# Optimization experiments

Hardware: AMD Instinct MI355X
Metric: run time of the kernel (lower is better)

Reference implementation:

```python
import jax, jax.numpy as jnp
import numpy as np

B, C, S, DC, P, VOCAB = 32, 2048, 512, 128, 768, 32000
CHARS_PER_SUB = C // S  # contiguous non-overlapping spans, no zero-width offsets


def setup_inputs() -> dict:
    key = jax.random.key(0)
    k1, k2, k3 = jax.random.split(key, 3)
    char_sequences = jax.random.randint(k1, (B, C), 0, VOCAB, dtype=jnp.int64 if jax.config.jax_enable_x64 else jnp.int32)
    # offsets[b, p] = (start, end) char span of subword p: contiguous spans of width 4
    starts = jnp.arange(S, dtype=jnp.int32) * CHARS_PER_SUB
    ends = starts + CHARS_PER_SUB
    offsets = jnp.broadcast_to(jnp.stack([starts, ends], axis=-1), (B, S, 2))
    char_table = jax.random.normal(k2, (VOCAB, DC), dtype=jnp.float32)
    pretrained_embeddings = jax.random.normal(k3, (B, S, P), dtype=jnp.float32)
    return {
        "char_sequences": char_sequences,
        "offsets": offsets,
        "char_table": char_table,
        "pretrained_embeddings": pretrained_embeddings,
    }


def _scatter_subword_to_chars(starts, ends, sub):
    # starts, ends: [S]; sub: [S, P]. For char position k, find p with start<=k<end.
    pos = jnp.arange(C)
    idx = jnp.clip(jnp.searchsorted(starts, pos, side="right") - 1, 0, starts.shape[0] - 1)
    valid = (pos >= starts[idx]) & (pos < ends[idx])  # positions not covered get zeros
    return jnp.where(valid[:, None], sub[idx], jnp.zeros((), sub.dtype))  # [C, P]


def reference(char_sequences, offsets, char_table, pretrained_embeddings):
    # character embedding lookup (dropout p=0.0 is identity)
    char_emb = char_table[char_sequences]  # [B, C, DC]
    scattered = jax.vmap(_scatter_subword_to_chars)(
        offsets[..., 0], offsets[..., 1], pretrained_embeddings
    )  # [B, C, P]
    return jnp.concatenate([char_emb, scattered], axis=-1)  # [B, C, DC+P]
```

## Files before the change

kernel.cpp:

```cpp
#include <hip/hip_runtime.h>
#include <stdint.h>

#define SCAT_THREADS (32u * 512u * 192u)
#define CHAR_CHUNKS  (32u * 2048u * 32u)

typedef float f32x4 __attribute__((ext_vector_type(4)));

__global__ __launch_bounds__(256) void EmbeddingLayer_14516989460967_kernel(
    const int*   __restrict__ seq,
    const int*   __restrict__ offsets,
    const float* __restrict__ table,
    const float* __restrict__ pret,
    float*       __restrict__ out)
{
    uint32_t gtid = blockIdx.x * 256u + threadIdx.x;

    if (gtid < SCAT_THREADS) {
        uint32_t sp  = gtid / 192u;
        uint32_t ck  = gtid - sp * 192u;
        int2 se = *(const int2*)(offsets + (sp << 1));
        f32x4 v = *(const f32x4*)(pret + (size_t)sp * 768u + (ck << 2));
        uint32_t b  = sp >> 9;
        uint32_t c0 = (sp & 511u) << 2;
        float* dst = out + ((size_t)((b << 11) + c0)) * 896u + 128u + (ck << 2);
        const f32x4 z = {0.f, 0.f, 0.f, 0.f};
#pragma unroll
        for (int j = 0; j < 4; ++j) {
            int c = (int)c0 + j;
            f32x4 w = (c >= se.x && c < se.y) ? v : z;
            *(f32x4*)(dst + (size_t)j * 896u) = w;
        }
    } else {
        uint32_t cid = gtid - SCAT_THREADS;
        uint32_t row = cid >> 5;
        uint32_t col = (cid & 31u) << 2;
        int tok = seq[row];
        f32x4 v = *(const f32x4*)(table + (size_t)tok * 128u + col);
        *(f32x4*)(out + (size_t)row * 896u + col) = v;
    }
}

extern "C" void kernel_launch(void* const* d_in, const int* in_sizes, int n_in,
                              void* d_out, int out_size, void* d_ws, size_t ws_size,
                              hipStream_t stream) {
    const int*   seq     = (const int*)  d_in[0];
    const int*   offsets = (const int*)  d_in[1];
    const float* table   = (const float*)d_in[2];
    const float* pret    = (const float*)d_in[3];

    uint32_t total_threads = SCAT_THREADS + CHAR_CHUNKS;
    uint32_t blocks = total_threads / 256u;
    EmbeddingLayer_14516989460967_kernel<<<blocks, 256, 0, stream>>>(
        seq, offsets, table, pret, (float*)d_out);
}
```

Before: 54.27 us.

## Assign each block a contiguous 16-row output tile covering both segments

Each block now handles 16 consecutive output rows (4 subwords) and writes both the char-embedding columns and the scattered subword columns for them, instead of two separate thread ranges writing the two segments in distant parts of the grid. The aim is to make each block's writes cover whole contiguous rows so DRAM write locality improves, and to cut the block count. Each thread now does more work (2 gather chunks plus 3 scatter chunks), so there is less parallelism to hide latency, and the block count is hardcoded to these sizes.

```diff
diff --git a/kernel.cpp b/kernel.cpp
--- a/kernel.cpp
+++ b/kernel.cpp
@@ -1,10 +1,10 @@
 #include <hip/hip_runtime.h>
 #include <stdint.h>
 
-#define SCAT_THREADS (32u * 512u * 192u)
-#define CHAR_CHUNKS  (32u * 2048u * 32u)
 
 typedef float f32x4 __attribute__((ext_vector_type(4)));
+
+#define NBLOCKS 4096u
 
 __global__ __launch_bounds__(256) void EmbeddingLayer_14516989460967_kernel(
     const int*   __restrict__ seq,
@@ -13,30 +13,37 @@
     const float* __restrict__ pret,
     float*       __restrict__ out)
 {
-    uint32_t gtid = blockIdx.x * 256u + threadIdx.x;
+    const uint32_t tid = threadIdx.x;
+    const uint32_t r0  = blockIdx.x * 16u;
+    const uint32_t sp0 = blockIdx.x * 4u;
 
-    if (gtid < SCAT_THREADS) {
-        uint32_t sp  = gtid / 192u;
-        uint32_t ck  = gtid - sp * 192u;
+#pragma unroll
+    for (uint32_t k = 0; k < 2u; ++k) {
+        uint32_t ci  = k * 256u + tid;
+        uint32_t row = r0 + (ci >> 5);
+        uint32_t col = (ci & 31u) << 2;
+        int tok = seq[row];
+        f32x4 v = *(const f32x4*)(table + (size_t)tok * 128u + col);
+        *(f32x4*)(out + (size_t)row * 896u + col) = v;
+    }
+
+#pragma unroll
+    for (uint32_t k = 0; k < 3u; ++k) {
+        uint32_t u  = k * 256u + tid;
+        uint32_t ls = u / 192u;
+        uint32_t ck = u - ls * 192u;
+        uint32_t sp = sp0 + ls;
         int2 se = *(const int2*)(offsets + (sp << 1));
         f32x4 v = *(const f32x4*)(pret + (size_t)sp * 768u + (ck << 2));
-        uint32_t b  = sp >> 9;
         uint32_t c0 = (sp & 511u) << 2;
-        float* dst = out + ((size_t)((b << 11) + c0)) * 896u + 128u + (ck << 2);
+        float* dst = out + (size_t)(r0 + (ls << 2)) * 896u + 128u + (ck << 2);
         const f32x4 z = {0.f, 0.f, 0.f, 0.f};
 #pragma unroll
-        for (int j = 0; j < 4; ++j) {
-            int c = (int)c0 + j;
+        for (uint32_t j = 0; j < 4u; ++j) {
+            int c = (int)(c0 + j);
             f32x4 w = (c >= se.x && c < se.y) ? v : z;
             *(f32x4*)(dst + (size_t)j * 896u) = w;
         }
-    } else {
-        uint32_t cid = gtid - SCAT_THREADS;
-        uint32_t row = cid >> 5;
-        uint32_t col = (cid & 31u) << 2;
-        int tok = seq[row];
-        f32x4 v = *(const f32x4*)(table + (size_t)tok * 128u + col);
-        *(f32x4*)(out + (size_t)row * 896u + col) = v;
     }
 }
 
@@ -48,8 +55,6 @@
     const float* table   = (const float*)d_in[2];
     const float* pret    = (const float*)d_in[3];
 
-    uint32_t total_threads = SCAT_THREADS + CHAR_CHUNKS;
-    uint32_t blocks = total_threads / 256u;
-    EmbeddingLayer_14516989460967_kernel<<<blocks, 256, 0, stream>>>(
+    EmbeddingLayer_14516989460967_kernel<<<NBLOCKS, 256, 0, stream>>>(
         seq, offsets, table, pret, (float*)d_out);
 }
```

After: 58.52 us. +7.8%, slower.
